# Kernel optimization log

Hardware: AMD Instinct MI355X
Metric: run time of the kernel (lower is better)

Reference implementation:

```python
import jax, jax.numpy as jnp
import numpy as np

B, DH, P, V, NP, K = 8, 1024, 64, 50257, 256, 8
SKEW = P * (P - 1) // 2


def setup_inputs() -> dict:
    key = jax.random.key(0)
    ks = jax.random.split(key, 24)
    f = jax.random.normal
    h_t = f(ks[0], (B, DH), jnp.float32)
    R = f(ks[1], (B, P, P), jnp.float32)
    A_t = 0.05 * (R - jnp.swapaxes(R, -1, -2))  # skew-symmetric
    B_t = f(ks[2], (B, NP, P), jnp.float32)
    E = f(ks[3], (V, P), jnp.float32)
    e_mask = f(ks[4], (B, P), jnp.float32)
    M = f(ks[5], (B, P, P), jnp.float32)
    G_tilde = jnp.eye(P) + 0.01 * jnp.einsum('bij,bkj->bik', M, M)  # SPD metric
    z0 = f(ks[6], (B, P), jnp.float32)
    s = lambda k_, sh: f(k_, sh, jnp.float32) * 0.02
    params = dict(
        WQ_w=s(ks[7], (DH, P)), WQ_b=jnp.zeros((P,)),
        WK_w=s(ks[8], (P, P)), WK_b=jnp.zeros((P,)),
        WV_w=s(ks[9], (P, P)), WV_b=jnp.zeros((P,)),
        WC_w=s(ks[10], (P, P)), WC_b=jnp.zeros((P,)),
        WO_w=s(ks[11], (DH, V)),
        WG_w=s(ks[12], (P, P)), WG_b=jnp.zeros((P,)),
        wgamma_w=s(ks[13], (DH + P + SKEW, 1)), wgamma_b=jnp.zeros((1,)),
        wmu_w=s(ks[14], (DH + P + 2, 1)), wmu_b=jnp.zeros((1,)),
        gdown_w=s(ks[15], (SKEW, P)),
        Sigma_inv=jnp.ones((P,)) * 0.1,
        hlie_w=s(ks[16], (DH, P)), hlie_b=jnp.zeros((P,)),
    )
    return dict(h_t=h_t, A_t=A_t, B_t=B_t, E=E, e_mask=e_mask,
                G_tilde=G_tilde, z0=z0, **params)


def _sq_riem(x, Y, G):
    # x: (B,p), Y: (B,n,p), G: (B,p,p) -> (B,n)
    d = Y - x[:, None, :]
    return jnp.einsum('bnp,bpq,bnq->bn', d, G, d)


def reference(h_t, A_t, B_t, E, e_mask, G_tilde, z0,
              WQ_w, WQ_b, WK_w, WK_b, WV_w, WV_b, WC_w, WC_b, WO_w,
              WG_w, WG_b, wgamma_w, wgamma_b, wmu_w, wmu_b,
              gdown_w, Sigma_inv, hlie_w, hlie_b):
    p = A_t.shape[-1]
    scale = 1.0 / jnp.sqrt(jnp.asarray(p, h_t.dtype))
    I = jnp.eye(p, dtype=A_t.dtype)
    Q_t = jnp.linalg.solve(I - A_t, jnp.broadcast_to(I + A_t, A_t.shape))  # Cayley map (B,p,p)
    q_t = h_t @ WQ_w + WQ_b                      # (B,p)
    B_rot = jnp.einsum('bnp,bpq->bnq', B_t, Q_t)  # (B,n,p)
    K_t = B_rot @ WK_w + WK_b
    V_t = B_rot @ WV_w + WV_b
    h_lie = h_t @ hlie_w + hlie_b                 # (B,p)
    omega = -0.5 * _sq_riem(h_lie, B_rot, G_tilde)  # (B,n)
    scores = jnp.einsum('bp,bnp->bn', q_t, K_t) * scale + omega
    alpha = jax.nn.softmax(scores, axis=-1)
    c_t = jnp.einsum('bn,bnp->bp', alpha, V_t)
    iu0, iu1 = jnp.triu_indices(p, k=1)
    g_t = A_t[:, iu0, iu1]                        # (B, skew_dim)
    E_gen = E @ WG_w + WG_b                       # (V,p)
    g_proj = g_t @ gdown_w                        # (B,p)
    diff = E_gen[None, :, :] - g_proj[:, None, :]  # (B,V,p)
    kappa = -jnp.sum(diff * diff * Sigma_inv, axis=-1)  # (B,V)
    base_logits = h_t @ WO_w                      # (B,V)
    c_rot = jnp.einsum('bp,bpq->bq', c_t @ WC_w + WC_b, Q_t)
    group_logits = c_rot @ E.T * scale + kappa
    gamma = jax.nn.sigmoid(jnp.concatenate([h_t, c_t, g_t], -1) @ wgamma_w + wgamma_b)
    logits = base_logits + gamma * group_logits
    pi = jax.nn.softmax(logits, axis=-1)
    topv, topi = jax.lax.top_k(pi, K)
    topp = topv / jnp.sum(topv, -1, keepdims=True)
    E_g = E[topi]                                 # (B,k,p) gather
    E_G = jnp.einsum('bkp,bpq->bkq', E_g, Q_t)
    E_exp = jnp.einsum('bk,bkp->bp', topp, E_G)
    H = -jnp.sum(pi * jnp.log(pi + 1e-12), -1, keepdims=True)
    rho = _sq_riem(h_lie, E_exp[:, None, :], G_tilde)  # (B,1)
    mu = jax.nn.sigmoid(jnp.concatenate([h_t, c_t, H, rho], -1) @ wmu_w + wmu_b)
    m_next = mu * e_mask + (1.0 - mu) * E_exp
    outer = m_next[:, :, None] * e_mask[:, None, :]
    A_next = A_t + 0.1 * (outer - jnp.swapaxes(outer, 1, 2))
    return logits, m_next, A_next
```

## Files before the change

### kernel.cpp

```cpp
#include <hip/hip_runtime.h>
#include <math.h>

#define NV    50257
#define OUT_M 402056
#define OUT_A 402568
#define SCALE 0.125f

#define WS_Q      0
#define WS_HTR    32768
#define WS_S      40960
#define WS_TV     45056
#define WS_C0     45120
#define WS_HLIE   47144
#define WS_W1     47656
#define WS_GH     48176
#define WS_WMAT   48192
#define WS_SC     80960
#define WS_WB     83008
#define WS_CONSTB 83520
#define WS_GAMMA  83528
#define WS_CT     83536
#define WS_P6     84048
#define WS_PQT    86016
#define WS_PHL    94208
#define WS_PGH    102400
#define WS_PGP    102528
#define WS_PGG    118912

__global__ __launch_bounds__(256) void kA_prep(
    const float* __restrict__ h_t, const float* __restrict__ A_t,
    const float* __restrict__ WG_w, const float* __restrict__ WG_b,
    const float* __restrict__ Sigma_inv,
    const float* __restrict__ WQ_w, const float* __restrict__ wgamma_w,
    const float* __restrict__ hlie_w, const float* __restrict__ gdown_w,
    float* __restrict__ ws)
{
    __shared__ float Ash[64][65];
    __shared__ float Gsh[64][65];
    __shared__ float hsh[1024];
    __shared__ float piv[2][132];
    __shared__ float fr[2][64];
    __shared__ float dsh[64];

    const int tid = threadIdx.x;
    const int blk = blockIdx.x;

    if (blk < 8) {
        const int b  = blk;
        const int i  = tid & 63;
        const int cb = __builtin_amdgcn_readfirstlane(tid >> 6);

        for (int idx = tid; idx < 4096; idx += 256)
            Ash[idx >> 6][idx & 63] = A_t[b*4096 + idx];
        for (int k = tid; k < 1024; k += 256)
            ws[WS_HTR + k*8 + b] = h_t[b*1024 + k];
        __syncthreads();

        float w[32];
        if (cb < 2) {
            #pragma unroll
            for (int jj = 0; jj < 32; ++jj) {
                int j = cb*32 + jj;
                w[jj] = (i == j ? 1.0f : 0.0f) - Ash[i][j];
            }
        } else {
            #pragma unroll
            for (int jj = 0; jj < 32; ++jj) {
                int j = (cb - 2)*32 + jj;
                w[jj] = (i == j ? 1.0f : 0.0f) + Ash[i][j];
            }
        }
        __syncthreads();

        #pragma unroll
        for (int k = 0; k < 64; ++k) {
            const int kb  = k >> 5;
            const int sel = k & 1;
            if (cb == kb) fr[sel][i] = w[k & 31];
            if (i == k) {
                #pragma unroll
                for (int q4 = 0; q4 < 8; ++q4)
                    *(float4*)&piv[sel][cb*32 + q4*4] =
                        make_float4(w[q4*4], w[q4*4+1], w[q4*4+2], w[q4*4+3]);
            }
            __syncthreads();
            float pk = piv[sel][k];
            float f = (i == k) ? 0.0f : (fr[sel][i] / pk);
            #pragma unroll
            for (int jj = 0; jj < 32; ++jj)
                w[jj] -= f * piv[sel][cb*32 + jj];
        }

        if (cb == (i >> 5)) dsh[i] = w[i & 31];
        __syncthreads();
        if (cb >= 2) {
            float dinv = 1.0f / dsh[i];
            #pragma unroll
            for (int jj = 0; jj < 32; ++jj)
                Ash[i][(cb - 2)*32 + jj] = w[jj] * dinv;
        }
        __syncthreads();
        for (int idx = tid; idx < 4096; idx += 256)
            ws[WS_Q + b*4096 + idx] = Ash[idx >> 6][idx & 63];
        return;
    }

    if (blk == 8) {
        const int a   = tid & 63;
        const int cb8 = __builtin_amdgcn_readfirstlane(tid >> 6);
        float* sig = hsh;
        float* bg  = hsh + 64;
        if (tid < 64) { sig[tid] = Sigma_inv[tid]; bg[tid] = WG_b[tid]; }
        __syncthreads();
        for (int idx = tid; idx < 4096; idx += 256) {
            int r = idx >> 6, c = idx & 63;
            float wv = WG_w[idx];
            Gsh[r][c] = wv;
            Ash[r][c] = wv * sig[c];
        }
        __syncthreads();
        float t8[16];
        #pragma unroll
        for (int j = 0; j < 16; ++j) t8[j] = 0.0f;
        for (int p = 0; p < 64; ++p) {
            float wv = Ash[a][p];
            #pragma unroll
            for (int jj = 0; jj < 16; ++jj) t8[jj] = fmaf(wv, Gsh[cb8*16 + jj][p], t8[jj]);
        }
        #pragma unroll
        for (int jj = 0; jj < 16; ++jj)
            ws[WS_S + a*64 + cb8*16 + jj] = t8[jj];
        if (cb8 == 0) {
            float s = 0.0f;
            for (int p = 0; p < 64; ++p) s += Ash[a][p] * bg[p];
            ws[WS_TV + a] = 2.0f * s;
        }
        if (tid == 0) {
            float c0 = 0.0f;
            for (int p = 0; p < 64; ++p) c0 += sig[p] * bg[p] * bg[p];
            ws[WS_C0] = c0;
        }
        return;
    }

    if (blk < 25) {
        const int c = blk - 9;
        const int i = tid & 63;
        const int w = __builtin_amdgcn_readfirstlane(tid >> 6);
        for (int idx = tid; idx < 4096; idx += 256) {
            int r = idx >> 6, col = idx & 63;
            int krow = c*64 + r;
            Ash[r][col] = WQ_w[krow*64 + col];
            Gsh[r][col] = hlie_w[krow*64 + col];
        }
        for (int t = tid; t < 512; t += 256) {
            int b = t >> 6, kk = t & 63;
            hsh[b*64 + kk] = h_t[b*1024 + c*64 + kk];
        }
        if (tid < 64) dsh[tid] = wgamma_w[c*64 + tid];
        __syncthreads();
        const int b0 = 2*w, b1 = 2*w + 1;
        float q0 = 0, q1 = 0, l0 = 0, l1 = 0;
        #pragma unroll 8
        for (int kk = 0; kk < 64; ++kk) {
            float a = Ash[kk][i], g = Gsh[kk][i];
            float h0 = hsh[b0*64 + kk], h1 = hsh[b1*64 + kk];
            q0 = fmaf(h0, a, q0); q1 = fmaf(h1, a, q1);
            l0 = fmaf(h0, g, l0); l1 = fmaf(h1, g, l1);
        }
        ws[WS_PQT + (c*8 + b0)*64 + i] = q0;
        ws[WS_PQT + (c*8 + b1)*64 + i] = q1;
        ws[WS_PHL + (c*8 + b0)*64 + i] = l0;
        ws[WS_PHL + (c*8 + b1)*64 + i] = l1;
        float g0 = hsh[b0*64 + i] * dsh[i];
        float g1 = hsh[b1*64 + i] * dsh[i];
        #pragma unroll
        for (int off = 32; off > 0; off >>= 1) {
            g0 += __shfl_xor(g0, off);
            g1 += __shfl_xor(g1, off);
        }
        if (i == 0) {
            ws[WS_PGH + c*8 + b0] = g0;
            ws[WS_PGH + c*8 + b1] = g1;
        }
        return;
    }

    {
        const int c = blk - 25;
        const int i = tid & 63;
        const int w = __builtin_amdgcn_readfirstlane(tid >> 6);
        for (int idx = tid; idx < 4032; idx += 256) {
            int r = idx >> 6, col = idx & 63;
            Ash[r][col] = gdown_w[(c*63 + r)*64 + col];
        }
        for (int t = tid; t < 504; t += 256) {
            int b = t / 63, sl = t % 63;
            int s = c*63 + sl;
            int i2 = 0, f = 0;
            while (f + (63 - i2) <= s) { f += 63 - i2; ++i2; }
            int j2 = i2 + 1 + (s - f);
            hsh[b*63 + sl] = A_t[b*4096 + i2*64 + j2];
        }
        if (tid < 63) dsh[tid] = wgamma_w[1088 + c*63 + tid];
        __syncthreads();
        const int b0 = 2*w, b1 = 2*w + 1;
        float a0 = 0, a1 = 0;
        #pragma unroll 4
        for (int sl = 0; sl < 63; ++sl) {
            float gd = Ash[sl][i];
            a0 = fmaf(hsh[b0*63 + sl], gd, a0);
            a1 = fmaf(hsh[b1*63 + sl], gd, a1);
        }
        ws[WS_PGP + (c*8 + b0)*64 + i] = a0;
        ws[WS_PGP + (c*8 + b1)*64 + i] = a1;
        float g0 = (i < 63) ? hsh[b0*63 + i] * dsh[i] : 0.0f;
        float g1 = (i < 63) ? hsh[b1*63 + i] * dsh[i] : 0.0f;
        #pragma unroll
        for (int off = 32; off > 0; off >>= 1) {
            g0 += __shfl_xor(g0, off);
            g1 += __shfl_xor(g1, off);
        }
        if (i == 0) {
            ws[WS_PGG + c*8 + b0] = g0;
            ws[WS_PGG + c*8 + b1] = g1;
        }
    }
}

__global__ __launch_bounds__(256) void kB_chain(
    const float* __restrict__ G_t,
    const float* __restrict__ WQ_b, const float* __restrict__ WK_w,
    const float* __restrict__ hlie_b,
    float* __restrict__ ws)
{
    __shared__ float Qsh[64][65], Gsh[64][65];
    __shared__ float part[4][64], partb[4][64];
    __shared__ float qt[64], hl[64], qkv[64], v0[64];
    __shared__ float red16[16];

    const int b = blockIdx.x, tid = threadIdx.x;
    const int i = tid & 63;
    const int cb = __builtin_amdgcn_readfirstlane(tid >> 6);
    const int col0 = cb * 16;

    for (int idx = tid; idx < 4096; idx += 256) {
        int r = idx >> 6, c = idx & 63;
        Qsh[r][c] = ws[WS_Q + b*4096 + idx];
        Gsh[r][c] = G_t[b*4096 + idx];
    }
    {
        float aq = 0, ah = 0;
        #pragma unroll
        for (int cc = 0; cc < 4; ++cc) {
            int c = cb*4 + cc;
            aq += ws[WS_PQT + (c*8 + b)*64 + i];
            ah += ws[WS_PHL + (c*8 + b)*64 + i];
        }
        part[cb][i] = aq; partb[cb][i] = ah;
    }
    if (tid < 16) red16[tid] = ws[WS_PGH + tid*8 + b];
    __syncthreads();
    if (tid < 64) {
        qt[tid] = part[0][tid]+part[1][tid]+part[2][tid]+part[3][tid] + WQ_b[tid];
        hl[tid] = partb[0][tid]+partb[1][tid]+partb[2][tid]+partb[3][tid] + hlie_b[tid];
    }
    if (tid == 0) {
        float s = 0;
        #pragma unroll
        for (int j = 0; j < 16; ++j) s += red16[j];
        ws[WS_GH + b] = s;
    }
    __syncthreads();
    {
        float acc = 0;
        #pragma unroll
        for (int jj = 0; jj < 16; ++jj)
            acc = fmaf(WK_w[i*64 + col0 + jj], qt[col0 + jj], acc);
        part[cb][i] = acc;
    }
    __syncthreads();
    if (tid < 64) qkv[tid] = part[0][tid]+part[1][tid]+part[2][tid]+part[3][tid];
    __syncthreads();
    {
        float acc = 0;
        #pragma unroll
        for (int jj = 0; jj < 16; ++jj)
            acc = fmaf(Gsh[i][col0 + jj], hl[col0 + jj], acc);
        part[cb][i] = acc;
    }
    __syncthreads();
    if (tid < 64)
        v0[tid] = SCALE*qkv[tid] + part[0][tid]+part[1][tid]+part[2][tid]+part[3][tid];
    __syncthreads();
    {
        float acc = 0;
        #pragma unroll
        for (int jj = 0; jj < 16; ++jj)
            acc = fmaf(Qsh[i][col0 + jj], v0[col0 + jj], acc);
        part[cb][i] = acc;
    }
    __syncthreads();
    if (tid < 64) {
        ws[WS_W1 + b*64 + tid]   = part[0][tid]+part[1][tid]+part[2][tid]+part[3][tid];
        ws[WS_HLIE + b*64 + tid] = hl[tid];
    }
    float tt[16];
    #pragma unroll
    for (int j = 0; j < 16; ++j) tt[j] = 0;
    for (int r = 0; r < 64; ++r) {
        float qv = Qsh[i][r];
        #pragma unroll
        for (int j = 0; j < 16; ++j) tt[j] = fmaf(qv, Gsh[r][col0 + j], tt[j]);
    }
    __syncthreads();
    #pragma unroll
    for (int j = 0; j < 16; ++j) Gsh[i][col0 + j] = tt[j];
    __syncthreads();
    float w2r[16];
    #pragma unroll
    for (int j = 0; j < 16; ++j) w2r[j] = 0;
    for (int q = 0; q < 64; ++q) {
        float tv = Gsh[i][q];
        #pragma unroll
        for (int j = 0; j < 16; ++j) w2r[j] = fmaf(tv, Qsh[col0 + j][q], w2r[j]);
    }
    #pragma unroll
    for (int j = 0; j < 16; ++j)
        ws[WS_WMAT + b*4096 + (col0 + j)*64 + i] = w2r[j];
}

__global__ __launch_bounds__(256) void kC_scores(
    const float* __restrict__ B_t, float* __restrict__ ws)
{
    __shared__ float Bsh[64][65];
    __shared__ float Wsh[64][64];
    __shared__ float w1sh[64];
    __shared__ float part[4][64];
    const int b = blockIdx.x >> 2, q4 = blockIdx.x & 3;
    const int tid = threadIdx.x, lane = tid & 63;
    const int gu = __builtin_amdgcn_readfirstlane(tid >> 6);
    const int col0 = gu * 16;
    for (int idx = tid; idx < 4096; idx += 256) {
        int r = idx >> 6, c = idx & 63;
        Bsh[r][c] = B_t[b*16384 + (q4*64 + r)*64 + c];
        Wsh[r][c] = ws[WS_WMAT + b*4096 + idx];
    }
    if (tid < 64) w1sh[tid] = ws[WS_W1 + b*64 + tid];
    __syncthreads();
    float t[16];
    #pragma unroll
    for (int j = 0; j < 16; ++j) t[j] = 0;
    for (int p = 0; p < 64; ++p) {
        float bv = Bsh[lane][p];
        #pragma unroll
        for (int j = 0; j < 16; ++j) t[j] = fmaf(bv, Wsh[p][col0 + j], t[j]);
    }
    float ps = 0;
    #pragma unroll
    for (int j = 0; j < 16; ++j) ps += (w1sh[col0+j] - 0.5f*t[j]) * Bsh[lane][col0+j];
    part[gu][lane] = ps;
    __syncthreads();
    if (tid < 64)
        ws[WS_SC + b*256 + q4*64 + tid] =
            part[0][tid]+part[1][tid]+part[2][tid]+part[3][tid];
}

__global__ __launch_bounds__(256) void kD_mid(
    const float* __restrict__ B_t,
    const float* __restrict__ WV_w, const float* __restrict__ WV_b,
    const float* __restrict__ WC_w, const float* __restrict__ WC_b,
    const float* __restrict__ WG_w, const float* __restrict__ WG_b,
    const float* __restrict__ wgamma_w, const float* __restrict__ wgamma_b,
    const float* __restrict__ Sigma_inv,
    float* __restrict__ ws)
{
    __shared__ float alpha[256], rr[256];
    __shared__ float part[4][64];
    __shared__ float cBr[64], cB[64], ct[64], cw[64], crot[64], gp[64], uv[64];
    __shared__ float red32[32];
    const int b = blockIdx.x, tid = threadIdx.x, lane = tid & 63;
    const int gu = __builtin_amdgcn_readfirstlane(tid >> 6);
    const int col0 = gu * 16;
    const float* Qb = ws + WS_Q + b*4096;

    float sv = ws[WS_SC + b*256 + tid];
    rr[tid] = sv;
    if (tid < 32) red32[tid] = ws[WS_PGG + tid*8 + b];
    __syncthreads();
    for (int off = 128; off > 0; off >>= 1) { if (tid < off) rr[tid] = fmaxf(rr[tid], rr[tid+off]); __syncthreads(); }
    float smax = rr[0]; __syncthreads();
    float e = expf(sv - smax);
    rr[tid] = e; __syncthreads();
    for (int off = 128; off > 0; off >>= 1) { if (tid < off) rr[tid] += rr[tid+off]; __syncthreads(); }
    float den = rr[0]; __syncthreads();
    alpha[tid] = e / den;
    __syncthreads();
    {
        float acc = 0;
        for (int nn = 0; nn < 64; ++nn) {
            int n = gu*64 + nn;
            acc = fmaf(alpha[n], B_t[b*16384 + n*64 + lane], acc);
        }
        part[gu][lane] = acc;
    }
    __syncthreads();
    if (tid < 64) cBr[tid] = part[0][tid]+part[1][tid]+part[2][tid]+part[3][tid];
    __syncthreads();
    {
        float acc = 0;
        #pragma unroll
        for (int pp = 0; pp < 16; ++pp) { int p = col0+pp; acc = fmaf(cBr[p], Qb[p*64+lane], acc); }
        part[gu][lane] = acc;
    }
    __syncthreads();
    if (tid < 64) cB[tid] = part[0][tid]+part[1][tid]+part[2][tid]+part[3][tid];
    __syncthreads();
    {
        float acc = 0;
        #pragma unroll
        for (int pp = 0; pp < 16; ++pp) { int p = col0+pp; acc = fmaf(cB[p], WV_w[p*64+lane], acc); }
        part[gu][lane] = acc;
    }
    __syncthreads();
    if (tid < 64) {
        float v = part[0][tid]+part[1][tid]+part[2][tid]+part[3][tid] + WV_b[tid];
        ct[tid] = v; ws[WS_CT + b*64 + tid] = v;
    }
    __syncthreads();
    {
        float acc = 0;
        #pragma unroll
        for (int pp = 0; pp < 16; ++pp) { int p = col0+pp; acc = fmaf(ct[p], WC_w[p*64+lane], acc); }
        part[gu][lane] = acc;
    }
    __syncthreads();
    if (tid < 64) cw[tid] = part[0][tid]+part[1][tid]+part[2][tid]+part[3][tid] + WC_b[tid];
    __syncthreads();
    {
        float acc = 0;
        #pragma unroll
        for (int pp = 0; pp < 16; ++pp) { int p = col0+pp; acc = fmaf(cw[p], Qb[p*64+lane], acc); }
        part[gu][lane] = acc;
    }
    __syncthreads();
    if (tid < 64) crot[tid] = part[0][tid]+part[1][tid]+part[2][tid]+part[3][tid];
    __syncthreads();
    {
        float acc = 0;
        #pragma unroll
        for (int cc = 0; cc < 8; ++cc) {
            int c = gu*8 + cc;
            acc += ws[WS_PGP + (c*8 + b)*64 + lane];
        }
        part[gu][lane] = acc;
    }
    if (tid < 64) rr[64 + tid] = ct[tid] * wgamma_w[1024 + tid];
    __syncthreads();
    if (tid < 64) {
        float g = part[0][tid]+part[1][tid]+part[2][tid]+part[3][tid];
        gp[tid] = g; uv[tid] = 2.0f * Sigma_inv[tid] * g;
    }
    if (tid == 0) {
        float gc = 0;
        for (int j = 0; j < 64; ++j) gc += rr[64 + j];
        float ga = 0;
        for (int j = 0; j < 32; ++j) ga += red32[j];
        float z = ws[WS_GH + b] + gc + ga + wgamma_b[0];
        ws[WS_GAMMA + b] = 1.0f / (1.0f + expf(-z));
    }
    __syncthreads();
    {
        float acc = 0;
        #pragma unroll
        for (int pp = 0; pp < 16; ++pp) { int p = col0+pp; acc = fmaf(WG_w[lane*64+p], uv[p], acc); }
        part[gu][lane] = acc;
    }
    if (tid < 64) rr[tid] = WG_b[tid]*uv[tid] - gp[tid]*gp[tid]*Sigma_inv[tid];
    __syncthreads();
    if (tid < 64)
        ws[WS_WB + b*64 + tid] = SCALE*crot[tid]
            + part[0][tid]+part[1][tid]+part[2][tid]+part[3][tid];
    if (tid == 0) { float s = 0; for (int j = 0; j < 64; ++j) s += rr[j]; ws[WS_CONSTB + b] = s; }
}

#define KU 16
__global__ __launch_bounds__(256) void k5_logits(
    const float* __restrict__ E, const float* __restrict__ WO_w,
    const float* __restrict__ ws, float* __restrict__ out)
{
    __shared__ float smem[11600];
    const int tid = threadIdx.x;
    const int q   = tid >> 6;
    const int vt  = tid & 63;
    const int vb  = blockIdx.x * 64;
    const int v   = vb + vt;
    const bool vok = v < NV;
    const int vv = vok ? v : NV - 1;

    float* Esh  = smem;
    float* Ssh  = smem + 4224;
    float* tvsh = smem + 8448;
    float* wbsh = smem + 8512;
    float* gmsh = smem + 9024;
    float* cbsh = smem + 9032;
    float* svsh = smem + 9040;
    float* gdsh = smem + 9296;
    float* accsh= smem + 9872;
    float* hsh  = smem;

    for (int idx = tid; idx < 1024; idx += 256) {
        int r = idx >> 4, c4 = (idx & 15) * 4;
        int vr = vb + r; if (vr >= NV) vr = NV - 1;
        float4 e4 = *(const float4*)(E + (size_t)vr * 64 + c4);
        float* dst = Esh + r*66 + c4;
        dst[0] = e4.x; dst[1] = e4.y; dst[2] = e4.z; dst[3] = e4.w;
    }
    for (int idx = tid; idx < 4096; idx += 256) Ssh[idx] = ws[WS_S + idx];
    for (int idx = tid; idx < 512; idx += 256) wbsh[idx] = ws[WS_WB + idx];
    if (tid < 64) tvsh[tid] = ws[WS_TV + tid];
    if (tid < 8) { gmsh[tid] = ws[WS_GAMMA + tid]; cbsh[tid] = ws[WS_CONSTB + tid]; }
    __syncthreads();
    {
        const float* er = Esh + vt*66;
        float sv = (q == 0) ? ws[WS_C0] : 0.0f;
        {
            float t[16];
            #pragma unroll
            for (int j = 0; j < 16; ++j) t[j] = 0.0f;
            for (int p = 0; p < 64; ++p) {
                float ep = er[p];
                #pragma unroll
                for (int j = 0; j < 16; ++j)
                    t[j] = fmaf(ep, Ssh[p*64 + q*16 + j], t[j]);
            }
            #pragma unroll
            for (int j = 0; j < 16; ++j)
                sv += (t[j] + tvsh[q*16 + j]) * er[q*16 + j];
        }
        svsh[q*64 + vt] = sv;
        const float* w0 = wbsh + (2*q    )*64;
        const float* w1 = wbsh + (2*q + 1)*64;
        float g0 = 0, g1 = 0;
        #pragma unroll 8
        for (int p = 0; p < 64; ++p) {
            float ep = er[p];
            g0 = fmaf(ep, w0[p], g0); g1 = fmaf(ep, w1[p], g1);
        }
        gdsh[vt*9 + 2*q]     = g0;
        gdsh[vt*9 + 2*q + 1] = g1;
    }
    __syncthreads();
    for (int idx = tid; idx < 2048; idx += 256)
        *(float4*)(hsh + idx*4) = *(const float4*)(ws + WS_HTR + idx*4);
    __syncthreads();
    float acc[8];
    #pragma unroll
    for (int bb = 0; bb < 8; ++bb) acc[bb] = 0.0f;
    {
        const float* wo = WO_w + (size_t)(q * 256) * NV + vv;
        const float* hb = hsh + q*256*8;
        for (int k0 = 0; k0 < 256; k0 += KU) {
            float wr[KU];
            #pragma unroll
            for (int u = 0; u < KU; ++u) wr[u] = wo[(size_t)(k0 + u) * NV];
            #pragma unroll
            for (int u = 0; u < KU; ++u) {
                const float* hp = hb + (k0 + u)*8;
                #pragma unroll
                for (int bb = 0; bb < 8; ++bb) acc[bb] = fmaf(hp[bb], wr[u], acc[bb]);
            }
        }
    }
    if (q) {
        float* ar = accsh + (q-1)*576 + vt*9;
        #pragma unroll
        for (int bb = 0; bb < 8; ++bb) ar[bb] = acc[bb];
    }
    __syncthreads();
    if (q == 0 && vok) {
        float svt = svsh[vt] + svsh[64+vt] + svsh[128+vt] + svsh[192+vt];
        const float* gr = gdsh + vt*9;
        #pragma unroll
        for (int bb = 0; bb < 8; ++bb) {
            float a = acc[bb] + accsh[vt*9+bb] + accsh[576+vt*9+bb] + accsh[1152+vt*9+bb];
            float gl = gr[bb] + cbsh[bb] - svt;
            out[bb*NV + v] = fmaf(gmsh[bb], gl, a);
        }
    }
}

#define NQ 12565
__global__ __launch_bounds__(256) void k6a_scan(
    const float* __restrict__ outl, float* __restrict__ ws)
{
    __shared__ float mvw[4][8];
    __shared__ int   miw[4][8];
    __shared__ float t8v[8];
    __shared__ int   t8i[8];
    __shared__ float redv[4], sred[4];
    const int b = blockIdx.x >> 2, qq = blockIdx.x & 3;
    const int tid = threadIdx.x, lane = tid & 63, wvi = tid >> 6;
    const int v0 = qq * NQ;
    const int v1 = (v0 + NQ < NV) ? (v0 + NQ) : NV;
    const float* lg = outl + b*NV;

    float lv[8]; int li[8];
    #pragma unroll
    for (int u = 0; u < 8; ++u) { lv[u] = -INFINITY; li[u] = 0x7fffffff; }
    float mt = -INFINITY, s1 = 0.0f, s2 = 0.0f;
    for (int v = v0 + tid; v < v1; v += 256) {
        float x = lg[v];
        if (x > mt) {
            float r = expf(mt - x);
            s1 *= r; s2 *= r; mt = x;
        }
        float ee = expf(x - mt);
        s1 += ee; s2 += x * ee;
        if (x > lv[7]) {
            float cv = x; int ci = v;
            #pragma unroll
            for (int u = 0; u < 8; ++u) {
                if (cv > lv[u]) {
                    float tv = lv[u]; lv[u] = cv; cv = tv;
                    int   ti = li[u]; li[u] = ci; ci = ti;
                }
            }
        }
    }
    float wv8[8]; int wi8[8];
    #pragma unroll
    for (int it = 0; it < 8; ++it) {
        float bv = lv[0]; int bi = li[0];
        #pragma unroll
        for (int off = 32; off > 0; off >>= 1) {
            float ov = __shfl_xor(bv, off);
            int   oi = __shfl_xor(bi, off);
            if (ov > bv || (ov == bv && oi < bi)) { bv = ov; bi = oi; }
        }
        wv8[it] = bv; wi8[it] = bi;
        if (lv[0] == bv && li[0] == bi) {
            lv[0]=lv[1]; lv[1]=lv[2]; lv[2]=lv[3]; lv[3]=lv[4];
            lv[4]=lv[5]; lv[5]=lv[6]; lv[6]=lv[7]; lv[7]=-INFINITY;
            li[0]=li[1]; li[1]=li[2]; li[2]=li[3]; li[3]=li[4];
            li[4]=li[5]; li[5]=li[6]; li[6]=li[7]; li[7]=0x7fffffff;
        }
    }
    if (lane == 0) {
        #pragma unroll
        for (int u = 0; u < 8; ++u) { mvw[wvi][u] = wv8[u]; miw[wvi][u] = wi8[u]; }
    }
    __syncthreads();
    if (tid == 0) {
        int pA = 0, pB = 0, pC = 0, pD = 0;
        for (int it = 0; it < 8; ++it) {
            float vA = mvw[0][pA], vB = mvw[1][pB], vC = mvw[2][pC], vD = mvw[3][pD];
            int   iA = miw[0][pA], iB = miw[1][pB], iC = miw[2][pC], iD = miw[3][pD];
            float best = vA; int bi = iA; int w = 0;
            if (vB > best || (vB == best && iB < bi)) { best = vB; bi = iB; w = 1; }
            if (vC > best || (vC == best && iC < bi)) { best = vC; bi = iC; w = 2; }
            if (vD > best || (vD == best && iD < bi)) { best = vD; bi = iD; w = 3; }
            t8v[it] = best; t8i[it] = bi;
            if (w == 0) ++pA; else if (w == 1) ++pB; else if (w == 2) ++pC; else ++pD;
        }
    }
    __syncthreads();
    float Mp = t8v[0];
    {
        float r = expf(mt - Mp);
        s1 *= r; s2 *= r;
    }
    #pragma unroll
    for (int off = 32; off > 0; off >>= 1) {
        s1 += __shfl_xor(s1, off);
        s2 += __shfl_xor(s2, off);
    }
    if (lane == 0) { redv[wvi] = s1; sred[wvi] = s2; }
    __syncthreads();
    if (tid == 0) {
        int base = WS_P6 + (b*4 + qq)*20;
        #pragma unroll
        for (int u = 0; u < 8; ++u) { ws[base + u] = t8v[u]; ((int*)ws)[base + 8 + u] = t8i[u]; }
        ws[base + 16] = Mp;
        ws[base + 17] = redv[0]+redv[1]+redv[2]+redv[3];
        ws[base + 18] = sred[0]+sred[1]+sred[2]+sred[3];
    }
}

__global__ __launch_bounds__(256) void k6b_final(
    const float* __restrict__ h_t, const float* __restrict__ A_t,
    const float* __restrict__ E, const float* __restrict__ e_mask,
    const float* __restrict__ G_t,
    const float* __restrict__ wmu_w, const float* __restrict__ wmu_b,
    const float* __restrict__ ws, float* __restrict__ out)
{
    __shared__ float mv[32];
    __shared__ int   mi[32];
    __shared__ float t8v[8];
    __shared__ int   t8i[8];
    __shared__ float toppsh[8];
    __shared__ float redv[256];
    __shared__ float uvec[64], eexp[64], msh[64], emsh[64];
    __shared__ float scal[4];
    const int b = blockIdx.x, tid = threadIdx.x;

    if (tid < 32) {
        int base = WS_P6 + (b*4 + (tid >> 3))*20;
        mv[tid] = ws[base + (tid & 7)];
        mi[tid] = ((const int*)ws)[base + 8 + (tid & 7)];
    }
    __syncthreads();
    if (tid == 0) {
        unsigned used = 0;
        for (int it = 0; it < 8; ++it) {
            float best = -INFINITY; int bi = 0x7fffffff, bs = 0;
            for (int c = 0; c < 32; ++c) {
                if (used & (1u << c)) continue;
                float x = mv[c];
                if (x > best || (x == best && mi[c] < bi)) { best = x; bi = mi[c]; bs = c; }
            }
            used |= 1u << bs; t8v[it] = best; t8i[it] = bi;
        }
        float M = t8v[0];
        float s1 = 0, s2 = 0;
        for (int q = 0; q < 4; ++q) {
            int base = WS_P6 + (b*4 + q)*20;
            float sc_ = expf(ws[base + 16] - M);
            s1 += ws[base + 17] * sc_; s2 += ws[base + 18] * sc_;
        }
        scal[0] = M + logf(s1) - s2 / s1;
        float ts = 0, tv_[8];
        #pragma unroll
        for (int u = 0; u < 8; ++u) { tv_[u] = expf(t8v[u] - M); ts += tv_[u]; }
        #pragma unroll
        for (int u = 0; u < 8; ++u) toppsh[u] = tv_[u] / ts;
    }
    __syncthreads();
    if (tid < 64) {
        float u_ = 0;
        #pragma unroll
        for (int j = 0; j < 8; ++j) u_ += toppsh[j] * E[t8i[j]*64 + tid];
        uvec[tid] = u_;
    }
    __syncthreads();
    if (tid < 64) {
        const float* Qb = ws + WS_Q + b*4096;
        float a = 0;
        for (int p = 0; p < 64; ++p) a += uvec[p] * Qb[p*64 + tid];
        eexp[tid] = a;
    }
    __syncthreads();
    {
        const float* Gb = G_t + b*4096;
        const float* HL = ws + WS_HLIE + b*64;
        float a = 0;
        #pragma unroll 4
        for (int t2 = 0; t2 < 16; ++t2) {
            int idx = tid*16 + t2;
            int p = idx >> 6, q = idx & 63;
            a += (eexp[p] - HL[p]) * Gb[idx] * (eexp[q] - HL[q]);
        }
        redv[tid] = a;
    }
    __syncthreads();
    for (int off = 128; off > 0; off >>= 1) {
        if (tid < off) redv[tid] += redv[tid + off];
        __syncthreads();
    }
    if (tid == 0) scal[1] = redv[0];
    __syncthreads();
    float pm = 0;
    for (int k = tid; k < 1024; k += 256) pm += h_t[b*1024 + k] * wmu_w[k];
    if (tid < 64) pm += ws[WS_CT + b*64 + tid] * wmu_w[1024 + tid];
    redv[tid] = pm;
    __syncthreads();
    for (int off = 128; off > 0; off >>= 1) {
        if (tid < off) redv[tid] += redv[tid + off];
        __syncthreads();
    }
    if (tid == 0) {
        float z = redv[0] + scal[0]*wmu_w[1088] + scal[1]*wmu_w[1089] + wmu_b[0];
        scal[2] = 1.0f / (1.0f + expf(-z));
    }
    __syncthreads();
    if (tid < 64) {
        float mu = scal[2];
        float em = e_mask[b*64 + tid];
        float m = mu*em + (1.0f - mu)*eexp[tid];
        out[OUT_M + b*64 + tid] = m;
        msh[tid] = m; emsh[tid] = em;
    }
    __syncthreads();
    for (int idx = tid; idx < 4096; idx += 256) {
        int i = idx >> 6, j = idx & 63;
        out[OUT_A + b*4096 + idx] = A_t[b*4096 + idx]
            + 0.1f*(msh[i]*emsh[j] - msh[j]*emsh[i]);
    }
}

extern "C" void kernel_launch(void* const* d_in, const int* in_sizes, int n_in,
                              void* d_out, int out_size, void* d_ws, size_t ws_size,
                              hipStream_t stream)
{
    const float* h_t      = (const float*)d_in[0];
    const float* A_t      = (const float*)d_in[1];
    const float* B_t      = (const float*)d_in[2];
    const float* E        = (const float*)d_in[3];
    const float* e_mask   = (const float*)d_in[4];
    const float* G_t      = (const float*)d_in[5];
    const float* WQ_w     = (const float*)d_in[7];
    const float* WQ_b     = (const float*)d_in[8];
    const float* WK_w     = (const float*)d_in[9];
    const float* WV_w     = (const float*)d_in[11];
    const float* WV_b     = (const float*)d_in[12];
    const float* WC_w     = (const float*)d_in[13];
    const float* WC_b     = (const float*)d_in[14];
    const float* WO_w     = (const float*)d_in[15];
    const float* WG_w     = (const float*)d_in[16];
    const float* WG_b     = (const float*)d_in[17];
    const float* wgamma_w = (const float*)d_in[18];
    const float* wgamma_b = (const float*)d_in[19];
    const float* wmu_w    = (const float*)d_in[20];
    const float* wmu_b    = (const float*)d_in[21];
    const float* gdown_w  = (const float*)d_in[22];
    const float* Sigma_inv= (const float*)d_in[23];
    const float* hlie_w   = (const float*)d_in[24];
    const float* hlie_b   = (const float*)d_in[25];
    float* out = (float*)d_out;
    float* ws  = (float*)d_ws;

    kA_prep<<<57, 256, 0, stream>>>(h_t, A_t, WG_w, WG_b, Sigma_inv,
                                    WQ_w, wgamma_w, hlie_w, gdown_w, ws);
    kB_chain<<<8, 256, 0, stream>>>(G_t, WQ_b, WK_w, hlie_b, ws);
    kC_scores<<<32, 256, 0, stream>>>(B_t, ws);
    kD_mid<<<8, 256, 0, stream>>>(B_t, WV_w, WV_b, WC_w, WC_b, WG_w, WG_b,
                                  wgamma_w, wgamma_b, Sigma_inv, ws);
    k5_logits<<<786, 256, 0, stream>>>(E, WO_w, ws, out);
    k6a_scan<<<32, 256, 0, stream>>>(out, ws);
    k6b_final<<<8, 256, 0, stream>>>(h_t, A_t, E, e_mask, G_t, wmu_w, wmu_b, ws, out);
}
```

Before: 524.5 us.

## Split logits kernel into group-logit pass and 8-way K-split WO GEMV

The fused logits kernel is split in two. The first kernel computes the group-logit term (E·S·E, E·wb, gamma scaling) for 128 vocab rows per block and stores it in workspace. The second runs the h_t @ WO_w GEMV with 32 columns per block and an 8-way K split, a shared-memory tree reduction, and launch bounds for higher occupancy. The aim is more blocks and more parallelism on the bandwidth-bound WO_w stream, at the cost of an extra launch and a workspace round trip for the group logits.

```diff
diff --git a/kernel.cpp b/kernel.cpp
--- a/kernel.cpp
+++ b/kernel.cpp
@@ -26,6 +26,7 @@
 #define WS_PGH    102400
 #define WS_PGP    102528
 #define WS_PGG    118912
+#define WS_GL     131072
 
 __global__ __launch_bounds__(256) void kA_prep(
     const float* __restrict__ h_t, const float* __restrict__ A_t,
@@ -484,32 +485,27 @@
     if (tid == 0) { float s = 0; for (int j = 0; j < 64; ++j) s += rr[j]; ws[WS_CONSTB + b] = s; }
 }
 
-#define KU 16
-__global__ __launch_bounds__(256) void k5_logits(
-    const float* __restrict__ E, const float* __restrict__ WO_w,
-    const float* __restrict__ ws, float* __restrict__ out)
+__global__ __launch_bounds__(256) void k5a_group(
+    const float* __restrict__ E, float* __restrict__ ws)
 {
-    __shared__ float smem[11600];
-    const int tid = threadIdx.x;
-    const int q   = tid >> 6;
-    const int vt  = tid & 63;
-    const int vb  = blockIdx.x * 64;
-    const int v   = vb + vt;
+    __shared__ float smem[14544];
+    const int tid  = threadIdx.x;
+    const int half = tid >> 7;
+    const int vt   = tid & 127;
+    const int vb = blockIdx.x * 128;
+    const int v = vb + vt;
     const bool vok = v < NV;
-    const int vv = vok ? v : NV - 1;
 
     float* Esh  = smem;
-    float* Ssh  = smem + 4224;
-    float* tvsh = smem + 8448;
-    float* wbsh = smem + 8512;
-    float* gmsh = smem + 9024;
-    float* cbsh = smem + 9032;
-    float* svsh = smem + 9040;
-    float* gdsh = smem + 9296;
-    float* accsh= smem + 9872;
-    float* hsh  = smem;
-
-    for (int idx = tid; idx < 1024; idx += 256) {
+    float* Ssh  = smem + 8448;
+    float* tvsh = smem + 12544;
+    float* wbsh = smem + 12608;
+    float* gmsh = smem + 13120;
+    float* cbsh = smem + 13128;
+    float* svsh = smem + 13136;
+    float* gdsh = smem + 13392;
+
+    for (int idx = tid; idx < 2048; idx += 256) {
         int r = idx >> 4, c4 = (idx & 15) * 4;
         int vr = vb + r; if (vr >= NV) vr = NV - 1;
         float4 e4 = *(const float4*)(E + (size_t)vr * 64 + c4);
@@ -523,8 +519,10 @@
     __syncthreads();
     {
         const float* er = Esh + vt*66;
-        float sv = (q == 0) ? ws[WS_C0] : 0.0f;
-        {
+        float sv = (half == 0) ? ws[WS_C0] : 0.0f;
+        #pragma unroll
+        for (int jj = 0; jj < 2; ++jj) {
+            const int jb = half*2 + jj;
             float t[16];
             #pragma unroll
             for (int j = 0; j < 16; ++j) t[j] = 0.0f;
@@ -532,61 +530,115 @@
                 float ep = er[p];
                 #pragma unroll
                 for (int j = 0; j < 16; ++j)
-                    t[j] = fmaf(ep, Ssh[p*64 + q*16 + j], t[j]);
+                    t[j] = fmaf(ep, Ssh[p*64 + jb*16 + j], t[j]);
             }
             #pragma unroll
             for (int j = 0; j < 16; ++j)
-                sv += (t[j] + tvsh[q*16 + j]) * er[q*16 + j];
-        }
-        svsh[q*64 + vt] = sv;
-        const float* w0 = wbsh + (2*q    )*64;
-        const float* w1 = wbsh + (2*q + 1)*64;
-        float g0 = 0, g1 = 0;
+                sv += (t[j] + tvsh[jb*16 + j]) * er[jb*16 + j];
+        }
+        svsh[half*128 + vt] = sv;
+        const float* w0 = wbsh + (half*4    )*64;
+        const float* w1 = wbsh + (half*4 + 1)*64;
+        const float* w2 = wbsh + (half*4 + 2)*64;
+        const float* w3 = wbsh + (half*4 + 3)*64;
+        float g0 = 0, g1 = 0, g2 = 0, g3 = 0;
         #pragma unroll 8
         for (int p = 0; p < 64; ++p) {
             float ep = er[p];
             g0 = fmaf(ep, w0[p], g0); g1 = fmaf(ep, w1[p], g1);
-        }
-        gdsh[vt*9 + 2*q]     = g0;
-        gdsh[vt*9 + 2*q + 1] = g1;
-    }
-    __syncthreads();
+            g2 = fmaf(ep, w2[p], g2); g3 = fmaf(ep, w3[p], g3);
+        }
+        float* gr = gdsh + vt*9 + half*4;
+        gr[0] = g0; gr[1] = g1; gr[2] = g2; gr[3] = g3;
+    }
+    __syncthreads();
+    if (half == 0 && vok) {
+        float svt = svsh[vt] + svsh[128 + vt];
+        const float* gr = gdsh + vt*9;
+        #pragma unroll
+        for (int bb = 0; bb < 8; ++bb)
+            ws[WS_GL + bb*NV + v] = gmsh[bb] * (gr[bb] + cbsh[bb] - svt);
+    }
+}
+
+#define KU5 16
+__global__ __launch_bounds__(256, 4) void k5b_wo(
+    const float* __restrict__ WO_w,
+    const float* __restrict__ ws, float* __restrict__ out)
+{
+    __shared__ float hsh[8192];
+    const int tid = threadIdx.x;
+    const int vt  = tid & 31;
+    const int kg  = tid >> 5;
+    const int vb  = blockIdx.x * 32;
+    const int v   = vb + vt;
+    const bool vok = v < NV;
+    const int vv = vok ? v : NV - 1;
+
     for (int idx = tid; idx < 2048; idx += 256)
         *(float4*)(hsh + idx*4) = *(const float4*)(ws + WS_HTR + idx*4);
     __syncthreads();
+
     float acc[8];
     #pragma unroll
     for (int bb = 0; bb < 8; ++bb) acc[bb] = 0.0f;
     {
-        const float* wo = WO_w + (size_t)(q * 256) * NV + vv;
-        const float* hb = hsh + q*256*8;
-        for (int k0 = 0; k0 < 256; k0 += KU) {
-            float wr[KU];
-            #pragma unroll
-            for (int u = 0; u < KU; ++u) wr[u] = wo[(size_t)(k0 + u) * NV];
-            #pragma unroll
-            for (int u = 0; u < KU; ++u) {
+        const float* wo = WO_w + (size_t)(kg * 128) * NV + vv;
+        const float* hb = hsh + kg*128*8;
+        for (int k0 = 0; k0 < 128; k0 += KU5) {
+            float wr[KU5];
+            #pragma unroll
+            for (int u = 0; u < KU5; ++u) wr[u] = wo[(size_t)(k0 + u) * NV];
+            #pragma unroll
+            for (int u = 0; u < KU5; ++u) {
                 const float* hp = hb + (k0 + u)*8;
                 #pragma unroll
                 for (int bb = 0; bb < 8; ++bb) acc[bb] = fmaf(hp[bb], wr[u], acc[bb]);
             }
         }
     }
-    if (q) {
-        float* ar = accsh + (q-1)*576 + vt*9;
-        #pragma unroll
-        for (int bb = 0; bb < 8; ++bb) ar[bb] = acc[bb];
-    }
-    __syncthreads();
-    if (q == 0 && vok) {
-        float svt = svsh[vt] + svsh[64+vt] + svsh[128+vt] + svsh[192+vt];
-        const float* gr = gdsh + vt*9;
-        #pragma unroll
-        for (int bb = 0; bb < 8; ++bb) {
-            float a = acc[bb] + accsh[vt*9+bb] + accsh[576+vt*9+bb] + accsh[1152+vt*9+bb];
-            float gl = gr[bb] + cbsh[bb] - svt;
-            out[bb*NV + v] = fmaf(gmsh[bb], gl, a);
-        }
+    float gl[8];
+    if (kg == 0) {
+        #pragma unroll
+        for (int bb = 0; bb < 8; ++bb) gl[bb] = ws[WS_GL + bb*NV + vv];
+    }
+    __syncthreads();
+    float* red = hsh;
+    if (kg >= 4) {
+        float* r = red + ((kg - 4)*32 + vt)*8;
+        #pragma unroll
+        for (int bb = 0; bb < 8; ++bb) r[bb] = acc[bb];
+    }
+    __syncthreads();
+    if (kg < 4) {
+        const float* r = red + (kg*32 + vt)*8;
+        #pragma unroll
+        for (int bb = 0; bb < 8; ++bb) acc[bb] += r[bb];
+    }
+    __syncthreads();
+    if (kg >= 2 && kg < 4) {
+        float* r = red + ((kg - 2)*32 + vt)*8;
+        #pragma unroll
+        for (int bb = 0; bb < 8; ++bb) r[bb] = acc[bb];
+    }
+    __syncthreads();
+    if (kg < 2) {
+        const float* r = red + (kg*32 + vt)*8;
+        #pragma unroll
+        for (int bb = 0; bb < 8; ++bb) acc[bb] += r[bb];
+    }
+    __syncthreads();
+    if (kg == 1) {
+        float* r = red + vt*8;
+        #pragma unroll
+        for (int bb = 0; bb < 8; ++bb) r[bb] = acc[bb];
+    }
+    __syncthreads();
+    if (kg == 0 && vok) {
+        const float* r = red + vt*8;
+        #pragma unroll
+        for (int bb = 0; bb < 8; ++bb)
+            out[bb*NV + v] = acc[bb] + r[bb] + gl[bb];
     }
 }
 
@@ -835,7 +887,8 @@
     kC_scores<<<32, 256, 0, stream>>>(B_t, ws);
     kD_mid<<<8, 256, 0, stream>>>(B_t, WV_w, WV_b, WC_w, WC_b, WG_w, WG_b,
                                   wgamma_w, wgamma_b, Sigma_inv, ws);
-    k5_logits<<<786, 256, 0, stream>>>(E, WO_w, ws, out);
+    k5a_group<<<393, 256, 0, stream>>>(E, ws);
+    k5b_wo<<<1571, 256, 0, stream>>>(WO_w, ws, out);
     k6a_scan<<<32, 256, 0, stream>>>(out, ws);
     k6b_final<<<8, 256, 0, stream>>>(h_t, A_t, E, e_mask, G_t, wmu_w, wmu_b, ws, out);
 }
```

After: 1.392 ms. 165% more time.
